# Performance work log

Hardware: AMD Instinct MI355X
Metric: run time of the kernel (lower is better)

Reference implementation:

```python
import jax, jax.numpy as jnp
import numpy as np

N = 10000          # num_stations / nodes
E = 320000         # edges
IN_DIM = 32
HID = 64
SEQ = 168
OUT_DIM = 10000


def _gcn_conv(x, W, b, src, dst, num_nodes):
    """PyG GCNConv: add self-loops, sym-normalize, gather-scatter aggregate."""
    loop = jnp.arange(num_nodes)
    s = jnp.concatenate([src, loop])
    d = jnp.concatenate([dst, loop])
    deg = jax.ops.segment_sum(jnp.ones_like(d, dtype=x.dtype), d, num_segments=num_nodes)
    dinv = jnp.where(deg > 0, jax.lax.rsqrt(deg), 0.0)
    norm = dinv[s] * dinv[d]                      # [E+N]
    h = x @ W.T                                   # [N, out] linear (no bias inside)
    msg = h[s] * norm[:, None]                    # gather + scale
    out = jax.ops.segment_sum(msg, d, num_segments=num_nodes)  # scatter-add
    return out + b


def setup_inputs() -> dict:
    key = jax.random.key(0)
    ks = jax.random.split(key, 16)
    sc = 0.05
    return {
        "x": jax.random.normal(ks[0], (N, IN_DIM), jnp.float32),
        "edge_index": jax.random.randint(ks[1], (2, E), 0, N, jnp.int64),
        "rain_history": jax.random.normal(ks[2], (1, SEQ), jnp.float32),
        "future_rain": jax.random.normal(ks[3], (1, 1), jnp.float32),
        "W1": jax.random.normal(ks[4], (HID, IN_DIM), jnp.float32) * sc,
        "b1": jnp.zeros((HID,), jnp.float32),
        "W2": jax.random.normal(ks[5], (HID, HID), jnp.float32) * sc,
        "b2": jnp.zeros((HID,), jnp.float32),
        "wf1_W": jax.random.normal(ks[6], (HID, SEQ + 1), jnp.float32) * sc,
        "wf1_b": jnp.zeros((HID,), jnp.float32),
        "wf2_W": jax.random.normal(ks[7], (HID, HID), jnp.float32) * sc,
        "wf2_b": jnp.zeros((HID,), jnp.float32),
        "of1_W": jax.random.normal(ks[8], (HID * 2, HID * N + HID), jnp.float32) * 0.001,
        "of1_b": jnp.zeros((HID * 2,), jnp.float32),
        "of2_W": jax.random.normal(ks[9], (OUT_DIM, HID * 2), jnp.float32) * sc,
        "of2_b": jnp.zeros((OUT_DIM,), jnp.float32),
    }


def reference(x, edge_index, rain_history, future_rain,
              W1, b1, W2, b2, wf1_W, wf1_b, wf2_W, wf2_b,
              of1_W, of1_b, of2_W, of2_b):
    src, dst = edge_index[0], edge_index[1]
    num_nodes = x.shape[0]
    h = jax.nn.relu(_gcn_conv(x, W1, b1, src, dst, num_nodes))
    h = jax.nn.relu(_gcn_conv(h, W2, b2, src, dst, num_nodes))
    h = jnp.clip(h, -10.0, 10.0)
    node_features = h.reshape(1, -1)                        # [1, N*HID]
    weather_input = jnp.concatenate([rain_history, future_rain], axis=1)  # [1, SEQ+1]
    w = jax.nn.relu(weather_input @ wf1_W.T + wf1_b)
    weather_features = w @ wf2_W.T + wf2_b                  # [1, HID]
    combined = jnp.concatenate([node_features, weather_features], axis=1)
    o = jax.nn.relu(combined @ of1_W.T + of1_b)
    out = o @ of2_W.T + of2_b                               # [1, OUT_DIM]
    return out.squeeze(0)
```

## Files before the change

kernel.cpp:

```cpp
#include <hip/hip_runtime.h>
#include <hip/hip_bf16.h>

#define N_NODES 10000
#define N_EDGES 320000
#define HID 64
#define IN_DIM 32
#define SEQ 168
#define OUT_DIM 10000
#define OF1_COLS 640064
#define OF1_NV   160016
#define OF1_SPLITS 24

typedef __attribute__((ext_vector_type(4))) float f32x4;

__global__ __launch_bounds__(256) void k_deg(const int* __restrict__ eidx, int* __restrict__ cnt) {
    int e = blockIdx.x * 256 + threadIdx.x;
    if (e < N_EDGES) atomicAdd(&cnt[eidx[N_EDGES + e]], 1);
}

__global__ __launch_bounds__(256) void k_scan(const int* __restrict__ cnt, int* __restrict__ row_start,
                                              float* __restrict__ dinv) {
    __shared__ int sums[256];
    const int CH = 40;
    int t = threadIdx.x;
    int base = t * CH;
    int s = 0;
    for (int i = 0; i < CH; i++) {
        int idx = base + i;
        if (idx < N_NODES) s += cnt[idx];
    }
    sums[t] = s;
    __syncthreads();
    for (int off = 1; off < 256; off <<= 1) {
        int v = sums[t];
        int add = (t >= off) ? sums[t - off] : 0;
        __syncthreads();
        sums[t] = v + add;
        __syncthreads();
    }
    int ex = (t == 0) ? 0 : sums[t - 1];
    for (int i = 0; i < CH; i++) {
        int idx = base + i;
        if (idx < N_NODES) {
            row_start[idx] = ex;
            int c = cnt[idx];
            ex += c;
            dinv[idx] = rsqrtf((float)(c + 1));
        }
    }
    if (t == 255) row_start[N_NODES] = ex;
}

__global__ __launch_bounds__(256) void k_fill(const int* __restrict__ eidx, const int* __restrict__ row_start,
                                              int* __restrict__ cursor, int* __restrict__ csr_src) {
    int e = blockIdx.x * 256 + threadIdx.x;
    if (e >= N_EDGES) return;
    int s = eidx[e];
    int d = eidx[N_EDGES + e];
    int slot = row_start[d] + atomicAdd(&cursor[d], 1);
    csr_src[slot] = s;
}

__global__ __launch_bounds__(256) void k_lin1(const float* __restrict__ x, const float* __restrict__ W,
                                              float* __restrict__ hlin) {
    __shared__ float Wl[64][33];
    __shared__ float xs[4][32];
    int t = threadIdx.x;
    for (int i = t; i < 64 * 32; i += 256) Wl[i >> 5][i & 31] = W[i];
    int node0 = blockIdx.x * 4;
    if (t < 128) {
        int n = t >> 5, k = t & 31;
        xs[n][k] = x[(node0 + n) * IN_DIM + k];
    }
    __syncthreads();
    int nl = t >> 6, j = t & 63;
    float acc = 0.f;
#pragma unroll
    for (int k = 0; k < 32; k++) acc += xs[nl][k] * Wl[j][k];
    hlin[(node0 + nl) * HID + j] = acc;
}

__global__ __launch_bounds__(256) void k_lin2(const float* __restrict__ h1, const float* __restrict__ W,
                                              float* __restrict__ hlin) {
    __shared__ float Wl[64][65];
    __shared__ float xs[4][64];
    int t = threadIdx.x;
    for (int i = t; i < 64 * 64; i += 256) Wl[i >> 6][i & 63] = W[i];
    int node0 = blockIdx.x * 4;
    int nl = t >> 6, j = t & 63;
    xs[nl][j] = h1[(node0 + nl) * HID + j];
    __syncthreads();
    float acc = 0.f;
#pragma unroll
    for (int k = 0; k < 64; k++) acc += xs[nl][k] * Wl[j][k];
    hlin[(node0 + nl) * HID + j] = acc;
}

__global__ __launch_bounds__(256) void k_agg(const float* __restrict__ hlin, const float* __restrict__ dinv,
                                             const int* __restrict__ row_start, const int* __restrict__ csr_src,
                                             const float* __restrict__ bias, float* __restrict__ out, int doClip) {
    int wave = (blockIdx.x * 256 + threadIdx.x) >> 6;
    int lane = threadIdx.x & 63;
    if (wave >= N_NODES) return;
    float dn = dinv[wave];
    float acc = hlin[wave * HID + lane] * dn * dn;
    int beg = row_start[wave], end = row_start[wave + 1];
    int k = beg;
    int s_next = (k < end) ? csr_src[k] : 0;
    while (k < end) {
        int s = s_next;
        k++;
        if (k < end) s_next = csr_src[k];
        acc += hlin[s * HID + lane] * (dinv[s] * dn);
    }
    float v = acc + bias[lane];
    v = fmaxf(v, 0.f);
    if (doClip) v = fminf(v, 10.f);
    out[wave * HID + lane] = v;
}

__global__ __launch_bounds__(64) void k_weather(const float* __restrict__ rain, const float* __restrict__ fut,
                                                const float* __restrict__ w1W, const float* __restrict__ w1b,
                                                const float* __restrict__ w2W, const float* __restrict__ w2b,
                                                float* __restrict__ comb) {
    __shared__ float wi[SEQ + 1];
    __shared__ float w1[64];
    int t = threadIdx.x;
    for (int i = t; i < SEQ; i += 64) wi[i] = rain[i];
    if (t == 0) wi[SEQ] = fut[0];
    __syncthreads();
    float acc = w1b[t];
    for (int i = 0; i < SEQ + 1; i++) acc += w1W[t * (SEQ + 1) + i] * wi[i];
    w1[t] = fmaxf(acc, 0.f);
    __syncthreads();
    float acc2 = w2b[t];
#pragma unroll
    for (int i = 0; i < 64; i++) acc2 += w2W[t * 64 + i] * w1[i];
    comb[HID * N_NODES + t] = acc2;
}

__global__ __launch_bounds__(256) void k_of1(const float* __restrict__ W, const float* __restrict__ comb,
                                             float* __restrict__ o_pre) {
    int j = blockIdx.y;
    int split = blockIdx.x;
    const int per = (OF1_NV + OF1_SPLITS - 1) / OF1_SPLITS;
    int i0 = split * per;
    int i1 = i0 + per;
    if (i1 > OF1_NV) i1 = OF1_NV;
    const f32x4* Wr = (const f32x4*)(W + (size_t)j * OF1_COLS);
    const f32x4* Cr = (const f32x4*)comb;
    float acc = 0.f;
    for (int i = i0 + threadIdx.x; i < i1; i += 256) {
        f32x4 wv = Wr[i];
        f32x4 cv = Cr[i];
        acc += wv.x * cv.x + wv.y * cv.y + wv.z * cv.z + wv.w * cv.w;
    }
#pragma unroll
    for (int off = 1; off < 64; off <<= 1) acc += __shfl_xor(acc, off, 64);
    __shared__ float red[4];
    int lane = threadIdx.x & 63, wid = threadIdx.x >> 6;
    if (lane == 0) red[wid] = acc;
    __syncthreads();
    if (threadIdx.x == 0) atomicAdd(&o_pre[j], red[0] + red[1] + red[2] + red[3]);
}

__global__ __launch_bounds__(256) void k_of2(const float* __restrict__ W, const float* __restrict__ of2b,
                                             const float* __restrict__ o_pre, const float* __restrict__ of1b,
                                             float* __restrict__ out) {
    __shared__ float os[128];
    int t = threadIdx.x;
    if (t < 128) os[t] = fmaxf(o_pre[t] + of1b[t], 0.f);
    __syncthreads();
    int k = blockIdx.x * 256 + t;
    if (k >= OUT_DIM) return;
    const f32x4* Wr = (const f32x4*)(W + (size_t)k * 128);
    float acc = of2b[k];
#pragma unroll
    for (int i = 0; i < 32; i++) {
        f32x4 wv = Wr[i];
        int base = i * 4;
        acc += wv.x * os[base + 0] + wv.y * os[base + 1] + wv.z * os[base + 2] + wv.w * os[base + 3];
    }
    out[k] = acc;
}

extern "C" void kernel_launch(void* const* d_in, const int* in_sizes, int n_in,
                              void* d_out, int out_size, void* d_ws, size_t ws_size,
                              hipStream_t stream) {
    const float* x    = (const float*)d_in[0];
    const int*  eidx  = (const int*)d_in[1];
    const float* rain = (const float*)d_in[2];
    const float* fut  = (const float*)d_in[3];
    const float* W1   = (const float*)d_in[4];
    const float* b1   = (const float*)d_in[5];
    const float* W2   = (const float*)d_in[6];
    const float* b2   = (const float*)d_in[7];
    const float* wf1W = (const float*)d_in[8];
    const float* wf1b = (const float*)d_in[9];
    const float* wf2W = (const float*)d_in[10];
    const float* wf2b = (const float*)d_in[11];
    const float* of1W = (const float*)d_in[12];
    const float* of1b = (const float*)d_in[13];
    const float* of2W = (const float*)d_in[14];
    const float* of2b = (const float*)d_in[15];
    float* out = (float*)d_out;

    char* p = (char*)d_ws;
    int*   cnt       = (int*)(p + 0);
    int*   row_start = (int*)(p + 40960);
    int*   cursor    = (int*)(p + 81920);
    float* dinv      = (float*)(p + 122880);
    int*   csr_src   = (int*)(p + 163840);
    float* hlin      = (float*)(p + 1474560);
    float* h1        = (float*)(p + 4194304);
    float* comb      = (float*)(p + 6815744);
    float* o_pre     = (float*)(p + 9437184);

    hipMemsetAsync(cnt, 0, N_NODES * sizeof(int), stream);
    hipMemsetAsync(cursor, 0, N_NODES * sizeof(int), stream);
    hipMemsetAsync(o_pre, 0, 128 * sizeof(float), stream);

    k_deg<<<(N_EDGES + 255) / 256, 256, 0, stream>>>(eidx, cnt);
    k_scan<<<1, 256, 0, stream>>>(cnt, row_start, dinv);
    k_fill<<<(N_EDGES + 255) / 256, 256, 0, stream>>>(eidx, row_start, cursor, csr_src);

    k_lin1<<<N_NODES / 4, 256, 0, stream>>>(x, W1, hlin);
    k_agg<<<N_NODES / 4, 256, 0, stream>>>(hlin, dinv, row_start, csr_src, b1, h1, 0);
    k_lin2<<<N_NODES / 4, 256, 0, stream>>>(h1, W2, hlin);
    k_agg<<<N_NODES / 4, 256, 0, stream>>>(hlin, dinv, row_start, csr_src, b2, comb, 1);

    k_weather<<<1, 64, 0, stream>>>(rain, fut, wf1W, wf1b, wf2W, wf2b, comb);

    k_of1<<<dim3(OF1_SPLITS, 128), 256, 0, stream>>>(of1W, comb, o_pre);
    k_of2<<<(OUT_DIM + 255) / 256, 256, 0, stream>>>(of2W, of2b, o_pre, of1b, out);
}
```

Baseline: 622.7 us.

## Fold degree norm into linear layers, batch of1 rows, split weather tail

Pre-scales the linear outputs by dinv so aggregation needs only one final scale, and loads neighbour indices cooperatively with wave shuffles. k_of1 now computes four output rows per block, sharing the activation loads, and uses nontemporal loads for the large weight matrix. The weather-feature contribution to of1 is computed separately in the small weather kernel. The three memsets are merged into one. These changes reduce redundant memory traffic and latency chains, at the cost of more register pressure in the of1 kernel.

```diff
diff --git a/kernel.cpp b/kernel.cpp
--- a/kernel.cpp
+++ b/kernel.cpp
@@ -8,8 +8,10 @@
 #define SEQ 168
 #define OUT_DIM 10000
 #define OF1_COLS 640064
-#define OF1_NV   160016
-#define OF1_SPLITS 24
+#define NODE_COLS 640000
+#define NODE_NV   160000
+#define OF1_SPLITS 64
+#define OF1_CHUNK  2500
 
 typedef __attribute__((ext_vector_type(4))) float f32x4;
 
@@ -62,7 +64,7 @@
 }
 
 __global__ __launch_bounds__(256) void k_lin1(const float* __restrict__ x, const float* __restrict__ W,
-                                              float* __restrict__ hlin) {
+                                              const float* __restrict__ dinv, float* __restrict__ hlin) {
     __shared__ float Wl[64][33];
     __shared__ float xs[4][32];
     int t = threadIdx.x;
@@ -77,11 +79,11 @@
     float acc = 0.f;
 #pragma unroll
     for (int k = 0; k < 32; k++) acc += xs[nl][k] * Wl[j][k];
-    hlin[(node0 + nl) * HID + j] = acc;
+    hlin[(node0 + nl) * HID + j] = acc * dinv[node0 + nl];
 }
 
 __global__ __launch_bounds__(256) void k_lin2(const float* __restrict__ h1, const float* __restrict__ W,
-                                              float* __restrict__ hlin) {
+                                              const float* __restrict__ dinv, float* __restrict__ hlin) {
     __shared__ float Wl[64][65];
     __shared__ float xs[4][64];
     int t = threadIdx.x;
@@ -93,7 +95,7 @@
     float acc = 0.f;
 #pragma unroll
     for (int k = 0; k < 64; k++) acc += xs[nl][k] * Wl[j][k];
-    hlin[(node0 + nl) * HID + j] = acc;
+    hlin[(node0 + nl) * HID + j] = acc * dinv[node0 + nl];
 }
 
 __global__ __launch_bounds__(256) void k_agg(const float* __restrict__ hlin, const float* __restrict__ dinv,
@@ -102,18 +104,19 @@
     int wave = (blockIdx.x * 256 + threadIdx.x) >> 6;
     int lane = threadIdx.x & 63;
     if (wave >= N_NODES) return;
-    float dn = dinv[wave];
-    float acc = hlin[wave * HID + lane] * dn * dn;
+    float acc = hlin[wave * HID + lane];
     int beg = row_start[wave], end = row_start[wave + 1];
-    int k = beg;
-    int s_next = (k < end) ? csr_src[k] : 0;
-    while (k < end) {
-        int s = s_next;
-        k++;
-        if (k < end) s_next = csr_src[k];
-        acc += hlin[s * HID + lane] * (dinv[s] * dn);
-    }
-    float v = acc + bias[lane];
+    for (int base = beg; base < end; base += 64) {
+        int idx = base + lane;
+        int sv = csr_src[(idx < end) ? idx : beg];
+        int m = end - base;
+        if (m > 64) m = 64;
+        for (int j = 0; j < m; j++) {
+            int s = __shfl(sv, j, 64);
+            acc += hlin[s * HID + lane];
+        }
+    }
+    float v = dinv[wave] * acc + bias[lane];
     v = fmaxf(v, 0.f);
     if (doClip) v = fminf(v, 10.f);
     out[wave * HID + lane] = v;
@@ -122,9 +125,10 @@
 __global__ __launch_bounds__(64) void k_weather(const float* __restrict__ rain, const float* __restrict__ fut,
                                                 const float* __restrict__ w1W, const float* __restrict__ w1b,
                                                 const float* __restrict__ w2W, const float* __restrict__ w2b,
-                                                float* __restrict__ comb) {
+                                                const float* __restrict__ of1W, float* __restrict__ wtail) {
     __shared__ float wi[SEQ + 1];
     __shared__ float w1[64];
+    __shared__ float wf[64];
     int t = threadIdx.x;
     for (int i = t; i < SEQ; i += 64) wi[i] = rain[i];
     if (t == 0) wi[SEQ] = fut[0];
@@ -136,40 +140,64 @@
     float acc2 = w2b[t];
 #pragma unroll
     for (int i = 0; i < 64; i++) acc2 += w2W[t * 64 + i] * w1[i];
-    comb[HID * N_NODES + t] = acc2;
+    wf[t] = acc2;
+    __syncthreads();
+#pragma unroll
+    for (int rr = 0; rr < 2; rr++) {
+        int r = t + rr * 64;
+        const float* Wt = of1W + (size_t)r * OF1_COLS + NODE_COLS;
+        float s = 0.f;
+#pragma unroll
+        for (int w = 0; w < 64; w++) s += Wt[w] * wf[w];
+        wtail[r] = s;
+    }
 }
 
 __global__ __launch_bounds__(256) void k_of1(const float* __restrict__ W, const float* __restrict__ comb,
                                              float* __restrict__ o_pre) {
-    int j = blockIdx.y;
     int split = blockIdx.x;
-    const int per = (OF1_NV + OF1_SPLITS - 1) / OF1_SPLITS;
-    int i0 = split * per;
-    int i1 = i0 + per;
-    if (i1 > OF1_NV) i1 = OF1_NV;
-    const f32x4* Wr = (const f32x4*)(W + (size_t)j * OF1_COLS);
-    const f32x4* Cr = (const f32x4*)comb;
-    float acc = 0.f;
+    int j0 = blockIdx.y * 4;
+    int i0 = split * OF1_CHUNK;
+    int i1 = i0 + OF1_CHUNK;
+    const f32x4* C4 = (const f32x4*)comb;
+    const f32x4* W0 = (const f32x4*)(W + (size_t)(j0 + 0) * OF1_COLS);
+    const f32x4* W1 = (const f32x4*)(W + (size_t)(j0 + 1) * OF1_COLS);
+    const f32x4* W2 = (const f32x4*)(W + (size_t)(j0 + 2) * OF1_COLS);
+    const f32x4* W3 = (const f32x4*)(W + (size_t)(j0 + 3) * OF1_COLS);
+    float a0 = 0.f, a1 = 0.f, a2 = 0.f, a3 = 0.f;
     for (int i = i0 + threadIdx.x; i < i1; i += 256) {
-        f32x4 wv = Wr[i];
-        f32x4 cv = Cr[i];
-        acc += wv.x * cv.x + wv.y * cv.y + wv.z * cv.z + wv.w * cv.w;
-    }
-#pragma unroll
-    for (int off = 1; off < 64; off <<= 1) acc += __shfl_xor(acc, off, 64);
-    __shared__ float red[4];
+        f32x4 cv = C4[i];
+        f32x4 w0 = __builtin_nontemporal_load(&W0[i]);
+        f32x4 w1 = __builtin_nontemporal_load(&W1[i]);
+        f32x4 w2 = __builtin_nontemporal_load(&W2[i]);
+        f32x4 w3 = __builtin_nontemporal_load(&W3[i]);
+        a0 += w0.x * cv.x + w0.y * cv.y + w0.z * cv.z + w0.w * cv.w;
+        a1 += w1.x * cv.x + w1.y * cv.y + w1.z * cv.z + w1.w * cv.w;
+        a2 += w2.x * cv.x + w2.y * cv.y + w2.z * cv.z + w2.w * cv.w;
+        a3 += w3.x * cv.x + w3.y * cv.y + w3.z * cv.z + w3.w * cv.w;
+    }
+#pragma unroll
+    for (int off = 1; off < 64; off <<= 1) {
+        a0 += __shfl_xor(a0, off, 64);
+        a1 += __shfl_xor(a1, off, 64);
+        a2 += __shfl_xor(a2, off, 64);
+        a3 += __shfl_xor(a3, off, 64);
+    }
+    __shared__ float red[4][4];
     int lane = threadIdx.x & 63, wid = threadIdx.x >> 6;
-    if (lane == 0) red[wid] = acc;
-    __syncthreads();
-    if (threadIdx.x == 0) atomicAdd(&o_pre[j], red[0] + red[1] + red[2] + red[3]);
+    if (lane == 0) { red[wid][0] = a0; red[wid][1] = a1; red[wid][2] = a2; red[wid][3] = a3; }
+    __syncthreads();
+    if (threadIdx.x < 4)
+        atomicAdd(&o_pre[j0 + threadIdx.x],
+                  red[0][threadIdx.x] + red[1][threadIdx.x] + red[2][threadIdx.x] + red[3][threadIdx.x]);
 }
 
 __global__ __launch_bounds__(256) void k_of2(const float* __restrict__ W, const float* __restrict__ of2b,
                                              const float* __restrict__ o_pre, const float* __restrict__ of1b,
-                                             float* __restrict__ out) {
+                                             const float* __restrict__ wtail, float* __restrict__ out) {
     __shared__ float os[128];
     int t = threadIdx.x;
-    if (t < 128) os[t] = fmaxf(o_pre[t] + of1b[t], 0.f);
+    if (t < 128) os[t] = fmaxf(o_pre[t] + of1b[t] + wtail[t], 0.f);
     __syncthreads();
     int k = blockIdx.x * 256 + t;
     if (k >= OUT_DIM) return;
@@ -177,7 +205,7 @@
     float acc = of2b[k];
 #pragma unroll
     for (int i = 0; i < 32; i++) {
-        f32x4 wv = Wr[i];
+        f32x4 wv = __builtin_nontemporal_load(&Wr[i]);
         int base = i * 4;
         acc += wv.x * os[base + 0] + wv.y * os[base + 1] + wv.z * os[base + 2] + wv.w * os[base + 3];
     }
@@ -207,30 +235,29 @@
 
     char* p = (char*)d_ws;
     int*   cnt       = (int*)(p + 0);
-    int*   row_start = (int*)(p + 40960);
-    int*   cursor    = (int*)(p + 81920);
+    int*   cursor    = (int*)(p + 40000);
+    float* o_pre     = (float*)(p + 80000);
+    int*   row_start = (int*)(p + 81920);
     float* dinv      = (float*)(p + 122880);
     int*   csr_src   = (int*)(p + 163840);
     float* hlin      = (float*)(p + 1474560);
     float* h1        = (float*)(p + 4194304);
     float* comb      = (float*)(p + 6815744);
-    float* o_pre     = (float*)(p + 9437184);
-
-    hipMemsetAsync(cnt, 0, N_NODES * sizeof(int), stream);
-    hipMemsetAsync(cursor, 0, N_NODES * sizeof(int), stream);
-    hipMemsetAsync(o_pre, 0, 128 * sizeof(float), stream);
+    float* wfeatT    = (float*)(p + 9437184);
+
+    hipMemsetAsync(p, 0, 80512, stream);
 
     k_deg<<<(N_EDGES + 255) / 256, 256, 0, stream>>>(eidx, cnt);
     k_scan<<<1, 256, 0, stream>>>(cnt, row_start, dinv);
     k_fill<<<(N_EDGES + 255) / 256, 256, 0, stream>>>(eidx, row_start, cursor, csr_src);
 
-    k_lin1<<<N_NODES / 4, 256, 0, stream>>>(x, W1, hlin);
+    k_lin1<<<N_NODES / 4, 256, 0, stream>>>(x, W1, dinv, hlin);
     k_agg<<<N_NODES / 4, 256, 0, stream>>>(hlin, dinv, row_start, csr_src, b1, h1, 0);
-    k_lin2<<<N_NODES / 4, 256, 0, stream>>>(h1, W2, hlin);
+    k_lin2<<<N_NODES / 4, 256, 0, stream>>>(h1, W2, dinv, hlin);
     k_agg<<<N_NODES / 4, 256, 0, stream>>>(hlin, dinv, row_start, csr_src, b2, comb, 1);
 
-    k_weather<<<1, 64, 0, stream>>>(rain, fut, wf1W, wf1b, wf2W, wf2b, comb);
-
-    k_of1<<<dim3(OF1_SPLITS, 128), 256, 0, stream>>>(of1W, comb, o_pre);
-    k_of2<<<(OUT_DIM + 255) / 256, 256, 0, stream>>>(of2W, of2b, o_pre, of1b, out);
-}
+    k_weather<<<1, 64, 0, stream>>>(rain, fut, wf1W, wf1b, wf2W, wf2b, of1W, wfeatT);
+
+    k_of1<<<dim3(OF1_SPLITS, 32), 256, 0, stream>>>(of1W, comb, o_pre);
+    k_of2<<<(OUT_DIM + 255) / 256, 256, 0, stream>>>(of2W, of2b, o_pre, of1b, wfeatT, out);
+}
```

Result: faster. 596.7 us (-4.2%).
